# Kernel optimization log

Hardware: AMD Instinct MI355X
Metric: run time of the kernel (lower is better)

## Reference

```python
import jax, jax.numpy as jnp
import numpy as np

B, T = 4096, 2048
CLIP = 1.0e5


def _hv(x):
    # smooth Heaviside: ~0 for x<0, ~1 for x>0
    return (jnp.tanh(5.0 * x) + 1.0) * 0.5


def setup_inputs() -> dict:
    key = jax.random.key(0)
    k1, _ = jax.random.split(key)
    # columns: prcp, tmean, dayl (all in [0,1) like normalized forcings)
    inputs = jax.random.uniform(k1, (B, T, 3), dtype=jnp.float32)
    # 15 scalar bucket parameters, all initialized to 0.5 as in build():
    # f, smax, qmax, ddf, tmin, tmax, Kc, SCmax, spmax, qpmax, kp, sgmax, qgmax, Kl, Kn
    theta = jnp.full((15,), 0.5, dtype=jnp.float32)
    return {"inputs": inputs, "theta": theta}


def _run(inputs, theta):
    f, smax, qmax, ddf, tmin, tmax, Kc, SCmax, spmax, qpmax, kp, sgmax, qgmax, Kl, Kn = [
        theta[i] for i in range(15)
    ]
    prcp = inputs[:, :, 0]   # [B,T]
    tmean = inputs[:, :, 1]
    dayl = inputs[:, :, 2]
    # Hamon-style PET computed once for the whole sequence
    pet = 29.8 * (dayl * 24.0) * 0.611 * jnp.exp(17.3 * tmean / (tmean + 237.3)) / (tmean + 273.2)

    # rescaled parameters (done once; constant over time)
    f_ = f / 10.0
    smax_ = smax * 1950.0
    qmax_ = qmax * 50.0
    ddf_ = ddf * 5.0
    tmin_ = tmin * -3.0
    tmax_ = tmax * 3.0
    Kc_ = Kc * 0.5
    SCmax_ = SCmax * 1.5
    spmax_ = spmax * 1950.0
    qpmax_ = qpmax * 40.0
    sgmax_ = sgmax * 1950.0
    qgmax_ = qgmax * 40.0
    Kl_ = Kl * 0.5
    Kn_ = Kn * 0.5
    Dc = 0.986 * 0.862

    def step(state, xt):
        s0, s1, s2, s3, s4 = [state[:, i] for i in range(5)]  # each [B]
        p, t, dl, pe = xt  # each [B]

        # canopy bucket
        day = _hv(dl - 0.5)
        night = _hv(0.5 - dl)
        scmax_t = day * SCmax_ * 2.0 + night * SCmax_ * 0.6
        lai_t = day * 0.478 + night * 0.15
        kc_t = day * Kc_ + night * Kc_ * 0.4
        pintc = (_hv(p - 0.1) * _hv(s0) * _hv(s0 - scmax_t) * p
                 + _hv(p - 0.1) * _hv(scmax_t - s0) * kc_t * Dc * lai_t)

        # rain/snow partition
        psnow = _hv(tmin_ - t) * p
        prain = _hv(t - tmin_) * p

        # snow bucket
        melt = _hv(t - tmax_) * _hv(s1) * jnp.minimum(s1, ddf_ * (t - tmax_))

        # preferential bucket
        qpref = (_hv(s2) * _hv(s2 - spmax_) * qpmax_
                 + _hv(s2) * _hv(spmax_ - s2) * kp * p * jnp.exp(-f_ * (spmax_ - s2)))

        # capillary (soil) bucket
        et = (_hv(s3) * _hv(s3 - smax_) * pe
              + _hv(s3) * _hv(smax_ - s3) * pe * (s3 / smax_))
        qsub = (_hv(s3) * _hv(s3 - smax_) * qmax_
                + _hv(s3) * _hv(smax_ - s3) * qmax_ * jnp.exp(-f_ * (smax_ - s3)))
        qout = _hv(s3) * _hv(s3 - smax_) * (s3 - smax_)

        # gravity bucket
        qslow = (_hv(s4) * _hv(s4 - sgmax_) * qgmax_
                 + _hv(s4) * _hv(sgmax_ - s4) * (p * Kl_ + p * p * Kn_) * jnp.exp(-f_ * (sgmax_ - s4)))

        ns0 = s0 + jnp.clip(pintc, -CLIP, CLIP)
        ns1 = s1 + jnp.clip(psnow - melt, -CLIP, CLIP)
        ns2 = s2 + jnp.clip(qpref, -CLIP, CLIP)
        ns3 = s3 + jnp.clip(prain + melt - et - qsub - qout, -CLIP, CLIP)
        ns4 = s4 + jnp.clip(qslow, -CLIP, CLIP)
        new_state = jnp.stack([ns0, ns1, ns2, ns3, ns4], axis=1)  # [B,5]
        return new_state, new_state

    init = jnp.zeros((inputs.shape[0], 5), dtype=inputs.dtype)
    xs = (prcp.T, tmean.T, dayl.T, pet.T)  # time-major [T,B]
    _, seq = jax.lax.scan(step, init, xs)  # seq: [T,B,5]
    return jnp.transpose(seq, (1, 0, 2))  # [B,T,5] state trajectories


def reference(inputs, theta):
    return _run(inputs, theta)
```

## Files before the change

kernel.cpp:

```cpp
#include <hip/hip_runtime.h>


#define NB 4096
#define NT 2048
#define CH 16
#define NCH (NT / CH)
#define CH23 32
#define BT ((size_t)NB * (size_t)NT)

#define L2E10 14.4269504089f
#define L2E    1.44269504089f

__device__ __forceinline__ float rcpf(float x) { return __builtin_amdgcn_rcpf(x); }
__device__ __forceinline__ float ex2(float a)  { return __builtin_amdgcn_exp2f(a); }
__device__ __forceinline__ float ex2c(float a) { return __builtin_amdgcn_exp2f(fminf(a, 80.0f)); }
__device__ __forceinline__ float clip1e5(float x) {
    return __builtin_amdgcn_fmed3f(x, -100000.0f, 100000.0f);
}
__device__ __forceinline__ void pinbuf(const float* d, int n4) {
    const float4* v = (const float4*)d;
    #pragma unroll
    for (int i = 0; i < n4; ++i)
        asm volatile("" :: "v"(v[i].x), "v"(v[i].y), "v"(v[i].z), "v"(v[i].w));
}

__global__ __launch_bounds__(64, 1)
void prnn_roles(const float* __restrict__ inp, const float* __restrict__ theta,
                float* __restrict__ out, float* __restrict__ wsp, int use_ws) {
    const int lane = threadIdx.x;
    const int role = blockIdx.x & 3;
    const int b = (blockIdx.x >> 2) * 64 + lane;

    const float f_     = theta[0] * 0.1f;
    const float smax_  = theta[1] * 1950.0f;
    const float qmax_  = theta[2] * 50.0f;
    const float ddf_   = theta[3] * 5.0f;
    const float tmin_  = theta[4] * -3.0f;
    const float tmax_  = theta[5] * 3.0f;
    const float Kc_    = theta[6] * 0.5f;
    const float SCmax_ = theta[7] * 1.5f;
    const float spmax_ = theta[8] * 1950.0f;
    const float qpmax_ = theta[9] * 40.0f;
    const float kp     = theta[10];
    const float sgmax_ = theta[11] * 1950.0f;
    const float qgmax_ = theta[12] * 40.0f;
    const float Kl_    = theta[13] * 0.5f;
    const float Kn_    = theta[14] * 0.5f;

    const float inv_smax = rcpf(smax_);
    const float KcDc  = Kc_ * 0.849932f;
    const float c_sn  = -L2E10 * tmin_;
    const float c_m   =  L2E10 * tmax_;
    const float c_dd  = -ddf_ * tmax_;
    const float c_sc1 =  L2E10 * SCmax_ * 1.4f;
    const float c_sc0 =  L2E10 * SCmax_ * 0.6f;
    const float c_2p  =  L2E10 * spmax_;
    const float c_3s  =  L2E10 * smax_;
    const float c_4s  =  L2E10 * sgmax_;
    const float fE    = f_ * L2E;
    const float c_E2  = -fE * spmax_;
    const float c_E3  = -fE * smax_;
    const float c_E4  = -fE * sgmax_;

    const float* ip = inp + (size_t)b * (NT * 3);
    float*       op = out + (size_t)b * (NT * 5);
    float* wbase = use_ws ? wsp : out;

    auto plane_storeN = [&](float* plane, const float* ob, int off, int n4) {
        float4* d = (float4*)(plane + (size_t)off);
        const float4* s = (const float4*)ob;
        #pragma unroll
        for (int i = 0; i < 8; ++i) { if (i < n4) d[i] = s[i]; }
    };

    if (role == 0) {
        float s0 = 0.f;
        float* w0 = wbase + 0 * BT + (size_t)b * NT;
        float bA[CH * 3], bB[CH * 3];
        auto pf = [&](float* d, int c) {
            const float4* s = (const float4*)(ip + (size_t)c * (CH * 3));
            #pragma unroll
            for (int i = 0; i < (CH * 3) / 4; ++i) ((float4*)d)[i] = s[i];
        };
        auto cw = [&](const float* d, int c) {
            float ob[CH];
            #pragma unroll
            for (int i = 0; i < CH; ++i) {
                const float p  = d[i * 3 + 0];
                const float dl = d[i * 3 + 2];
                const float day = rcpf(1.0f + ex2(fmaf(-L2E10, dl, 7.21347520f)));
                const float da  = 1.0f + ex2(fmaf(-L2E10, p, L2E));
                const float lai   = fmaf(0.328f, day, 0.15f);
                const float kcf   = fmaf(0.6f, day, 0.4f);
                const float kterm = KcDc * kcf * lai;
                const float zday  = fmaf(c_sc1, day, c_sc0);
                const float e0  = ex2(-L2E10 * s0);
                const float esc = ex2(fmaf(-L2E10, s0, zday));
                const float d0  = 1.0f + e0;
                const float dsc = 1.0f + esc;
                const float Rp  = rcpf(da * d0 * dsc);
                const float pintc = Rp * fmaf(d0 * esc, kterm, p);
                s0 += clip1e5(pintc);
                ob[i] = s0;
            }
            if (use_ws) plane_storeN(w0, ob, c * CH, CH / 4);
            else {
                #pragma unroll
                for (int i = 0; i < CH; ++i) op[(c * CH + i) * 5 + 0] = ob[i];
            }
        };
        pf(bA, 0);
        for (int c = 0; c < NCH; c += 2) {
            pf(bB, c + 1);
            pinbuf(bA, (CH * 3) / 4);
            cw(bA, c);
            if (c + 2 < NCH) pf(bA, c + 2);
            pinbuf(bB, (CH * 3) / 4);
            cw(bB, c + 1);
        }
    } else if (role == 1) {
        float s1 = 0.f, s3 = 0.f;
        float* w1 = wbase + 1 * BT + (size_t)b * NT;
        float* w3 = wbase + 3 * BT + (size_t)b * NT;
        float bA[CH * 3], bB[CH * 3];
        auto pf = [&](float* d, int c) {
            const float4* s = (const float4*)(ip + (size_t)c * (CH * 3));
            #pragma unroll
            for (int i = 0; i < (CH * 3) / 4; ++i) ((float4*)d)[i] = s[i];
        };
        auto cw = [&](const float* d, int c) {
            float ob1[CH], ob3[CH];
            #pragma unroll
            for (int i = 0; i < CH; ++i) {
                const float p  = d[i * 3 + 0];
                const float tm = d[i * 3 + 1];
                const float dl = d[i * 3 + 2];
                const float A1 = tm + 237.3f;
                const float A2 = tm + 273.2f;
                const float qq = rcpf(A1 * A2);
                const float pe = 436.98672f * dl * ex2(24.958624f * tm * (qq * A2)) * (qq * A1);
                const float psnow = rcpf(1.0f + ex2(fmaf(L2E10, tm, c_sn))) * p;
                const float dm = 1.0f + ex2(fmaf(-L2E10, tm, c_m));
                const float prain = p - psnow;
                const float e1 = ex2(-L2E10 * s1);
                const float melt = rcpf(dm * (1.0f + e1))
                                   * fminf(s1, fmaf(ddf_, tm, c_dd));
                const float e3  = ex2(-L2E10 * s3);
                const float e3s = ex2c(fmaf(-L2E10, s3, c_3s));
                const float R3  = rcpf((1.0f + e3) * (1.0f + e3s));
                const float E3  = ex2(fmaf(fE, s3, c_E3));
                const float t_et = pe * fmaf(e3s * s3, inv_smax, 1.0f);
                const float t_qs = qmax_ * fmaf(e3s, E3, 1.0f);
                const float outflux = R3 * (t_et + t_qs + (s3 - smax_));
                const float ds3 = prain + melt - outflux;
                s1 += clip1e5(psnow - melt);
                s3 += clip1e5(ds3);
                ob1[i] = s1;
                ob3[i] = s3;
            }
            if (use_ws) {
                plane_storeN(w1, ob1, c * CH, CH / 4);
                plane_storeN(w3, ob3, c * CH, CH / 4);
            } else {
                #pragma unroll
                for (int i = 0; i < CH; ++i) {
                    op[(c * CH + i) * 5 + 1] = ob1[i];
                    op[(c * CH + i) * 5 + 3] = ob3[i];
                }
            }
        };
        pf(bA, 0);
        for (int c = 0; c < NCH; c += 2) {
            pf(bB, c + 1);
            pinbuf(bA, (CH * 3) / 4);
            cw(bA, c);
            if (c + 2 < NCH) pf(bA, c + 2);
            pinbuf(bB, (CH * 3) / 4);
            cw(bB, c + 1);
        }
    } else if (role == 2) {
        float s2 = 0.f;
        float pA[CH23], pB[CH23];
        float* w2 = wbase + 2 * BT + (size_t)b * NT;
        auto pf = [&](float* P, int c) {
            #pragma unroll
            for (int i = 0; i < CH23; ++i) P[i] = ip[(c * CH23 + i) * 3 + 0];
        };
        auto cw = [&](const float* P, int c) {
            float ob[CH23];
            #pragma unroll
            for (int i = 0; i < CH23; ++i) {
                const float p = P[i];
                const float e2  = ex2(-L2E10 * s2);
                const float e2p = ex2c(fmaf(-L2E10, s2, c_2p));
                const float R2  = rcpf((1.0f + e2) * (1.0f + e2p));
                const float E2  = ex2(fmaf(fE, s2, c_E2));
                const float qpref = R2 * fmaf(e2p * E2, kp * p, qpmax_);
                s2 += clip1e5(qpref);
                ob[i] = s2;
            }
            if (use_ws) plane_storeN(w2, ob, c * CH23, CH23 / 4);
            else {
                #pragma unroll
                for (int i = 0; i < CH23; ++i) op[(c * CH23 + i) * 5 + 2] = ob[i];
            }
        };
        pf(pA, 0);
        for (int c = 0; c < NT / CH23; c += 2) {
            pf(pB, c + 1);
            pinbuf(pA, CH23 / 4);
            cw(pA, c);
            if (c + 2 < NT / CH23) pf(pA, c + 2);
            pinbuf(pB, CH23 / 4);
            cw(pB, c + 1);
        }
    } else {
        float s4 = 0.f;
        float pA[CH23], pB[CH23];
        float* w4 = wbase + 4 * BT + (size_t)b * NT;
        auto pf = [&](float* P, int c) {
            #pragma unroll
            for (int i = 0; i < CH23; ++i) P[i] = ip[(c * CH23 + i) * 3 + 0];
        };
        auto cw = [&](const float* P, int c) {
            float ob[CH23];
            #pragma unroll
            for (int i = 0; i < CH23; ++i) {
                const float p = P[i];
                const float e4  = ex2(-L2E10 * s4);
                const float e4s = ex2c(fmaf(-L2E10, s4, c_4s));
                const float R4  = rcpf((1.0f + e4) * (1.0f + e4s));
                const float E4  = ex2(fmaf(fE, s4, c_E4));
                const float pl  = p * fmaf(p, Kn_, Kl_);
                const float qslow = R4 * fmaf(e4s * E4, pl, qgmax_);
                s4 += clip1e5(qslow);
                ob[i] = s4;
            }
            if (use_ws) plane_storeN(w4, ob, c * CH23, CH23 / 4);
            else {
                #pragma unroll
                for (int i = 0; i < CH23; ++i) op[(c * CH23 + i) * 5 + 4] = ob[i];
            }
        };
        pf(pA, 0);
        for (int c = 0; c < NT / CH23; c += 2) {
            pf(pB, c + 1);
            pinbuf(pA, CH23 / 4);
            cw(pA, c);
            if (c + 2 < NT / CH23) pf(pA, c + 2);
            pinbuf(pB, CH23 / 4);
            cw(pB, c + 1);
        }
    }
}

__global__ __launch_bounds__(256)
void tx_kernel(const float* __restrict__ wsp, float* __restrict__ out) {
    const size_t idx = (size_t)blockIdx.x * 256 + threadIdx.x;
    const size_t b  = idx / (NT / 8);
    const size_t t0 = (idx % (NT / 8)) * 8;
    const float* base = wsp + b * NT + t0;
    float v[5][8];
    #pragma unroll
    for (int s = 0; s < 5; ++s) {
        *(float4*)&v[s][0] = *(const float4*)(base + s * BT);
        *(float4*)&v[s][4] = *(const float4*)(base + s * BT + 4);
    }
    float o[40];
    #pragma unroll
    for (int t = 0; t < 8; ++t)
        #pragma unroll
        for (int s = 0; s < 5; ++s) o[t * 5 + s] = v[s][t];
    float4* d = (float4*)(out + (b * NT + t0) * 5);
    const float4* sv = (const float4*)o;
    #pragma unroll
    for (int i = 0; i < 10; ++i) d[i] = sv[i];
}

extern "C" void kernel_launch(void* const* d_in, const int* in_sizes, int n_in,
                              void* d_out, int out_size, void* d_ws, size_t ws_size,
                              hipStream_t stream) {
    const float* inp   = (const float*)d_in[0];
    const float* theta = (const float*)d_in[1];
    float* out = (float*)d_out;
    float* wsp = (float*)d_ws;
    const int use_ws = (wsp != nullptr && ws_size >= 5 * sizeof(float) * BT) ? 1 : 0;
    prnn_roles<<<4 * (NB / 64), 64, 0, stream>>>(inp, theta, out, wsp, use_ws);
    if (use_ws)
        tx_kernel<<<(int)(BT / 8 / 256), 256, 0, stream>>>(wsp, out);
}
```

Measured before the change: 561.2 us.

## Process two batch rows per thread to interleave independent recurrences

Each thread now advances two independent batch rows' recurrences in lockstep, providing instruction-level parallelism to hide the latency of the serial exp/rcp chain. The grid is halved accordingly, and chunk sizes are unified to 8 timesteps with stores every two chunks. The trade-off is half as many wavefronts across the GPU, leaving many CUs idle, plus higher register pressure.

New measurement: 876.0 us. +56.1%, slower.

```diff
diff --git a/kernel.cpp b/kernel.cpp
--- a/kernel.cpp
+++ b/kernel.cpp
@@ -3,9 +3,8 @@
 
 #define NB 4096
 #define NT 2048
-#define CH 16
+#define CH 8
 #define NCH (NT / CH)
-#define CH23 32
 #define BT ((size_t)NB * (size_t)NT)
 
 #define L2E10 14.4269504089f
@@ -29,7 +28,8 @@
                 float* __restrict__ out, float* __restrict__ wsp, int use_ws) {
     const int lane = threadIdx.x;
     const int role = blockIdx.x & 3;
-    const int b = (blockIdx.x >> 2) * 64 + lane;
+    const int b0 = (blockIdx.x >> 2) * 128 + lane;
+    const int b1 = b0 + 64;
 
     const float f_     = theta[0] * 0.1f;
     const float smax_  = theta[1] * 1950.0f;
@@ -62,194 +62,273 @@
     const float c_E3  = -fE * smax_;
     const float c_E4  = -fE * sgmax_;
 
-    const float* ip = inp + (size_t)b * (NT * 3);
-    float*       op = out + (size_t)b * (NT * 5);
+    const float* ip0 = inp + (size_t)b0 * (NT * 3);
+    const float* ip1 = inp + (size_t)b1 * (NT * 3);
+    float*       op0 = out + (size_t)b0 * (NT * 5);
+    float*       op1 = out + (size_t)b1 * (NT * 5);
     float* wbase = use_ws ? wsp : out;
 
-    auto plane_storeN = [&](float* plane, const float* ob, int off, int n4) {
+    auto st16 = [&](float* plane, const float* ob, int off) {
         float4* d = (float4*)(plane + (size_t)off);
         const float4* s = (const float4*)ob;
         #pragma unroll
-        for (int i = 0; i < 8; ++i) { if (i < n4) d[i] = s[i]; }
+        for (int i = 0; i < 4; ++i) d[i] = s[i];
     };
 
     if (role == 0) {
-        float s0 = 0.f;
-        float* w0 = wbase + 0 * BT + (size_t)b * NT;
-        float bA[CH * 3], bB[CH * 3];
-        auto pf = [&](float* d, int c) {
-            const float4* s = (const float4*)(ip + (size_t)c * (CH * 3));
-            #pragma unroll
-            for (int i = 0; i < (CH * 3) / 4; ++i) ((float4*)d)[i] = s[i];
-        };
-        auto cw = [&](const float* d, int c) {
-            float ob[CH];
-            #pragma unroll
-            for (int i = 0; i < CH; ++i) {
-                const float p  = d[i * 3 + 0];
-                const float dl = d[i * 3 + 2];
-                const float day = rcpf(1.0f + ex2(fmaf(-L2E10, dl, 7.21347520f)));
-                const float da  = 1.0f + ex2(fmaf(-L2E10, p, L2E));
-                const float lai   = fmaf(0.328f, day, 0.15f);
-                const float kcf   = fmaf(0.6f, day, 0.4f);
-                const float kterm = KcDc * kcf * lai;
-                const float zday  = fmaf(c_sc1, day, c_sc0);
-                const float e0  = ex2(-L2E10 * s0);
-                const float esc = ex2(fmaf(-L2E10, s0, zday));
-                const float d0  = 1.0f + e0;
-                const float dsc = 1.0f + esc;
-                const float Rp  = rcpf(da * d0 * dsc);
-                const float pintc = Rp * fmaf(d0 * esc, kterm, p);
-                s0 += clip1e5(pintc);
-                ob[i] = s0;
-            }
-            if (use_ws) plane_storeN(w0, ob, c * CH, CH / 4);
+        float sa = 0.f, sb = 0.f;
+        float iA0[CH * 3], iA1[CH * 3], iB0[CH * 3], iB1[CH * 3];
+        float oa[2 * CH], ob[2 * CH];
+        float* w0a = wbase + 0 * BT + (size_t)b0 * NT;
+        float* w0b = wbase + 0 * BT + (size_t)b1 * NT;
+        auto pf = [&](float* d0, float* d1, int c) {
+            const float4* s0 = (const float4*)(ip0 + (size_t)c * (CH * 3));
+            const float4* s1 = (const float4*)(ip1 + (size_t)c * (CH * 3));
+            #pragma unroll
+            for (int i = 0; i < (CH * 3) / 4; ++i) {
+                ((float4*)d0)[i] = s0[i];
+                ((float4*)d1)[i] = s1[i];
+            }
+        };
+        auto cw = [&](const float* d0, const float* d1, int half) {
+            #pragma unroll
+            for (int i = 0; i < CH; ++i) {
+                const float p0 = d0[i * 3 + 0], p1 = d1[i * 3 + 0];
+                const float dl0 = d0[i * 3 + 2], dl1 = d1[i * 3 + 2];
+                const float dy0 = rcpf(1.0f + ex2(fmaf(-L2E10, dl0, 7.21347520f)));
+                const float dy1 = rcpf(1.0f + ex2(fmaf(-L2E10, dl1, 7.21347520f)));
+                const float da0 = 1.0f + ex2(fmaf(-L2E10, p0, L2E));
+                const float da1 = 1.0f + ex2(fmaf(-L2E10, p1, L2E));
+                const float la0 = fmaf(0.328f, dy0, 0.15f);
+                const float la1 = fmaf(0.328f, dy1, 0.15f);
+                const float kc0 = fmaf(0.6f, dy0, 0.4f);
+                const float kc1 = fmaf(0.6f, dy1, 0.4f);
+                const float kt0 = KcDc * kc0 * la0;
+                const float kt1 = KcDc * kc1 * la1;
+                const float zd0 = fmaf(c_sc1, dy0, c_sc0);
+                const float zd1 = fmaf(c_sc1, dy1, c_sc0);
+                const float e0a = ex2(-L2E10 * sa);
+                const float e0b = ex2(-L2E10 * sb);
+                const float ea  = ex2(fmaf(-L2E10, sa, zd0));
+                const float eb  = ex2(fmaf(-L2E10, sb, zd1));
+                const float d0a = 1.0f + e0a;
+                const float d0b = 1.0f + e0b;
+                const float dsa = 1.0f + ea;
+                const float dsb = 1.0f + eb;
+                const float Ra  = rcpf(da0 * d0a * dsa);
+                const float Rb  = rcpf(da1 * d0b * dsb);
+                const float pa  = Ra * fmaf(d0a * ea, kt0, p0);
+                const float pb  = Rb * fmaf(d0b * eb, kt1, p1);
+                sa += clip1e5(pa);
+                sb += clip1e5(pb);
+                oa[half * CH + i] = sa;
+                ob[half * CH + i] = sb;
+            }
+        };
+        pf(iA0, iA1, 0);
+        for (int c = 0; c < NCH; c += 2) {
+            pf(iB0, iB1, c + 1);
+            pinbuf(iA0, (CH * 3) / 4); pinbuf(iA1, (CH * 3) / 4);
+            cw(iA0, iA1, 0);
+            if (c + 2 < NCH) pf(iA0, iA1, c + 2);
+            pinbuf(iB0, (CH * 3) / 4); pinbuf(iB1, (CH * 3) / 4);
+            cw(iB0, iB1, 1);
+            if (use_ws) { st16(w0a, oa, c * CH); st16(w0b, ob, c * CH); }
             else {
                 #pragma unroll
-                for (int i = 0; i < CH; ++i) op[(c * CH + i) * 5 + 0] = ob[i];
-            }
-        };
-        pf(bA, 0);
-        for (int c = 0; c < NCH; c += 2) {
-            pf(bB, c + 1);
-            pinbuf(bA, (CH * 3) / 4);
-            cw(bA, c);
-            if (c + 2 < NCH) pf(bA, c + 2);
-            pinbuf(bB, (CH * 3) / 4);
-            cw(bB, c + 1);
+                for (int i = 0; i < 2 * CH; ++i) {
+                    op0[(c * CH + i) * 5 + 0] = oa[i];
+                    op1[(c * CH + i) * 5 + 0] = ob[i];
+                }
+            }
         }
     } else if (role == 1) {
-        float s1 = 0.f, s3 = 0.f;
-        float* w1 = wbase + 1 * BT + (size_t)b * NT;
-        float* w3 = wbase + 3 * BT + (size_t)b * NT;
-        float bA[CH * 3], bB[CH * 3];
-        auto pf = [&](float* d, int c) {
-            const float4* s = (const float4*)(ip + (size_t)c * (CH * 3));
-            #pragma unroll
-            for (int i = 0; i < (CH * 3) / 4; ++i) ((float4*)d)[i] = s[i];
-        };
-        auto cw = [&](const float* d, int c) {
-            float ob1[CH], ob3[CH];
-            #pragma unroll
-            for (int i = 0; i < CH; ++i) {
-                const float p  = d[i * 3 + 0];
-                const float tm = d[i * 3 + 1];
-                const float dl = d[i * 3 + 2];
-                const float A1 = tm + 237.3f;
-                const float A2 = tm + 273.2f;
-                const float qq = rcpf(A1 * A2);
-                const float pe = 436.98672f * dl * ex2(24.958624f * tm * (qq * A2)) * (qq * A1);
-                const float psnow = rcpf(1.0f + ex2(fmaf(L2E10, tm, c_sn))) * p;
-                const float dm = 1.0f + ex2(fmaf(-L2E10, tm, c_m));
-                const float prain = p - psnow;
-                const float e1 = ex2(-L2E10 * s1);
-                const float melt = rcpf(dm * (1.0f + e1))
-                                   * fminf(s1, fmaf(ddf_, tm, c_dd));
-                const float e3  = ex2(-L2E10 * s3);
-                const float e3s = ex2c(fmaf(-L2E10, s3, c_3s));
-                const float R3  = rcpf((1.0f + e3) * (1.0f + e3s));
-                const float E3  = ex2(fmaf(fE, s3, c_E3));
-                const float t_et = pe * fmaf(e3s * s3, inv_smax, 1.0f);
-                const float t_qs = qmax_ * fmaf(e3s, E3, 1.0f);
-                const float outflux = R3 * (t_et + t_qs + (s3 - smax_));
-                const float ds3 = prain + melt - outflux;
-                s1 += clip1e5(psnow - melt);
-                s3 += clip1e5(ds3);
-                ob1[i] = s1;
-                ob3[i] = s3;
-            }
+        float s1a = 0.f, s1b = 0.f, s3a = 0.f, s3b = 0.f;
+        float iA0[CH * 3], iA1[CH * 3], iB0[CH * 3], iB1[CH * 3];
+        float o1a[2 * CH], o1b[2 * CH], o3a[2 * CH], o3b[2 * CH];
+        float* w1a = wbase + 1 * BT + (size_t)b0 * NT;
+        float* w1b = wbase + 1 * BT + (size_t)b1 * NT;
+        float* w3a = wbase + 3 * BT + (size_t)b0 * NT;
+        float* w3b = wbase + 3 * BT + (size_t)b1 * NT;
+        auto pf = [&](float* d0, float* d1, int c) {
+            const float4* s0 = (const float4*)(ip0 + (size_t)c * (CH * 3));
+            const float4* s1 = (const float4*)(ip1 + (size_t)c * (CH * 3));
+            #pragma unroll
+            for (int i = 0; i < (CH * 3) / 4; ++i) {
+                ((float4*)d0)[i] = s0[i];
+                ((float4*)d1)[i] = s1[i];
+            }
+        };
+        auto cw = [&](const float* d0, const float* d1, int half) {
+            #pragma unroll
+            for (int i = 0; i < CH; ++i) {
+                const float p0 = d0[i * 3 + 0], p1 = d1[i * 3 + 0];
+                const float t0 = d0[i * 3 + 1], t1 = d1[i * 3 + 1];
+                const float l0 = d0[i * 3 + 2], l1 = d1[i * 3 + 2];
+                const float A1a = t0 + 237.3f, A1b = t1 + 237.3f;
+                const float A2a = t0 + 273.2f, A2b = t1 + 273.2f;
+                const float qa = rcpf(A1a * A2a);
+                const float qb = rcpf(A1b * A2b);
+                const float pea = 436.98672f * l0 * ex2(24.958624f * t0 * (qa * A2a)) * (qa * A1a);
+                const float peb = 436.98672f * l1 * ex2(24.958624f * t1 * (qb * A2b)) * (qb * A1b);
+                const float psa = rcpf(1.0f + ex2(fmaf(L2E10, t0, c_sn))) * p0;
+                const float psb = rcpf(1.0f + ex2(fmaf(L2E10, t1, c_sn))) * p1;
+                const float dma = 1.0f + ex2(fmaf(-L2E10, t0, c_m));
+                const float dmb = 1.0f + ex2(fmaf(-L2E10, t1, c_m));
+                const float pra = p0 - psa;
+                const float prb = p1 - psb;
+                const float e1a = ex2(-L2E10 * s1a);
+                const float e1b = ex2(-L2E10 * s1b);
+                const float mla = rcpf(dma * (1.0f + e1a)) * fminf(s1a, fmaf(ddf_, t0, c_dd));
+                const float mlb = rcpf(dmb * (1.0f + e1b)) * fminf(s1b, fmaf(ddf_, t1, c_dd));
+                const float e3a = ex2(-L2E10 * s3a);
+                const float e3b = ex2(-L2E10 * s3b);
+                const float ga  = ex2c(fmaf(-L2E10, s3a, c_3s));
+                const float gb  = ex2c(fmaf(-L2E10, s3b, c_3s));
+                const float Ra  = rcpf((1.0f + e3a) * (1.0f + ga));
+                const float Rb  = rcpf((1.0f + e3b) * (1.0f + gb));
+                const float Ea  = ex2(fmaf(fE, s3a, c_E3));
+                const float Eb  = ex2(fmaf(fE, s3b, c_E3));
+                const float ta_ = pea * fmaf(ga * s3a, inv_smax, 1.0f);
+                const float tb_ = peb * fmaf(gb * s3b, inv_smax, 1.0f);
+                const float ua  = qmax_ * fmaf(ga, Ea, 1.0f);
+                const float ub  = qmax_ * fmaf(gb, Eb, 1.0f);
+                const float ofa = Ra * (ta_ + ua + (s3a - smax_));
+                const float ofb = Rb * (tb_ + ub + (s3b - smax_));
+                const float d3a = pra + mla - ofa;
+                const float d3b = prb + mlb - ofb;
+                s1a += clip1e5(psa - mla);
+                s1b += clip1e5(psb - mlb);
+                s3a += clip1e5(d3a);
+                s3b += clip1e5(d3b);
+                o1a[half * CH + i] = s1a;
+                o1b[half * CH + i] = s1b;
+                o3a[half * CH + i] = s3a;
+                o3b[half * CH + i] = s3b;
+            }
+        };
+        pf(iA0, iA1, 0);
+        for (int c = 0; c < NCH; c += 2) {
+            pf(iB0, iB1, c + 1);
+            pinbuf(iA0, (CH * 3) / 4); pinbuf(iA1, (CH * 3) / 4);
+            cw(iA0, iA1, 0);
+            if (c + 2 < NCH) pf(iA0, iA1, c + 2);
+            pinbuf(iB0, (CH * 3) / 4); pinbuf(iB1, (CH * 3) / 4);
+            cw(iB0, iB1, 1);
             if (use_ws) {
-                plane_storeN(w1, ob1, c * CH, CH / 4);
-                plane_storeN(w3, ob3, c * CH, CH / 4);
+                st16(w1a, o1a, c * CH); st16(w1b, o1b, c * CH);
+                st16(w3a, o3a, c * CH); st16(w3b, o3b, c * CH);
             } else {
                 #pragma unroll
-                for (int i = 0; i < CH; ++i) {
-                    op[(c * CH + i) * 5 + 1] = ob1[i];
-                    op[(c * CH + i) * 5 + 3] = ob3[i];
+                for (int i = 0; i < 2 * CH; ++i) {
+                    op0[(c * CH + i) * 5 + 1] = o1a[i];
+                    op1[(c * CH + i) * 5 + 1] = o1b[i];
+                    op0[(c * CH + i) * 5 + 3] = o3a[i];
+                    op1[(c * CH + i) * 5 + 3] = o3b[i];
                 }
             }
-        };
-        pf(bA, 0);
-        for (int c = 0; c < NCH; c += 2) {
-            pf(bB, c + 1);
-            pinbuf(bA, (CH * 3) / 4);
-            cw(bA, c);
-            if (c + 2 < NCH) pf(bA, c + 2);
-            pinbuf(bB, (CH * 3) / 4);
-            cw(bB, c + 1);
         }
     } else if (role == 2) {
-        float s2 = 0.f;
-        float pA[CH23], pB[CH23];
-        float* w2 = wbase + 2 * BT + (size_t)b * NT;
-        auto pf = [&](float* P, int c) {
-            #pragma unroll
-            for (int i = 0; i < CH23; ++i) P[i] = ip[(c * CH23 + i) * 3 + 0];
-        };
-        auto cw = [&](const float* P, int c) {
-            float ob[CH23];
-            #pragma unroll
-            for (int i = 0; i < CH23; ++i) {
-                const float p = P[i];
-                const float e2  = ex2(-L2E10 * s2);
-                const float e2p = ex2c(fmaf(-L2E10, s2, c_2p));
-                const float R2  = rcpf((1.0f + e2) * (1.0f + e2p));
-                const float E2  = ex2(fmaf(fE, s2, c_E2));
-                const float qpref = R2 * fmaf(e2p * E2, kp * p, qpmax_);
-                s2 += clip1e5(qpref);
-                ob[i] = s2;
-            }
-            if (use_ws) plane_storeN(w2, ob, c * CH23, CH23 / 4);
+        float sa = 0.f, sb = 0.f;
+        float pA0[CH], pA1[CH], pB0[CH], pB1[CH];
+        float oa[2 * CH], ob[2 * CH];
+        float* w2a = wbase + 2 * BT + (size_t)b0 * NT;
+        float* w2b = wbase + 2 * BT + (size_t)b1 * NT;
+        auto pf = [&](float* P0, float* P1, int c) {
+            #pragma unroll
+            for (int i = 0; i < CH; ++i) {
+                P0[i] = ip0[(c * CH + i) * 3 + 0];
+                P1[i] = ip1[(c * CH + i) * 3 + 0];
+            }
+        };
+        auto cw = [&](const float* P0, const float* P1, int half) {
+            #pragma unroll
+            for (int i = 0; i < CH; ++i) {
+                const float p0 = P0[i], p1 = P1[i];
+                const float e2a = ex2(-L2E10 * sa);
+                const float e2b = ex2(-L2E10 * sb);
+                const float ga  = ex2c(fmaf(-L2E10, sa, c_2p));
+                const float gb  = ex2c(fmaf(-L2E10, sb, c_2p));
+                const float Ra  = rcpf((1.0f + e2a) * (1.0f + ga));
+                const float Rb  = rcpf((1.0f + e2b) * (1.0f + gb));
+                const float Ea  = ex2(fmaf(fE, sa, c_E2));
+                const float Eb  = ex2(fmaf(fE, sb, c_E2));
+                const float qa  = Ra * fmaf(ga * Ea, kp * p0, qpmax_);
+                const float qb  = Rb * fmaf(gb * Eb, kp * p1, qpmax_);
+                sa += clip1e5(qa);
+                sb += clip1e5(qb);
+                oa[half * CH + i] = sa;
+                ob[half * CH + i] = sb;
+            }
+        };
+        pf(pA0, pA1, 0);
+        for (int c = 0; c < NCH; c += 2) {
+            pf(pB0, pB1, c + 1);
+            pinbuf(pA0, CH / 4); pinbuf(pA1, CH / 4);
+            cw(pA0, pA1, 0);
+            if (c + 2 < NCH) pf(pA0, pA1, c + 2);
+            pinbuf(pB0, CH / 4); pinbuf(pB1, CH / 4);
+            cw(pB0, pB1, 1);
+            if (use_ws) { st16(w2a, oa, c * CH); st16(w2b, ob, c * CH); }
             else {
                 #pragma unroll
-                for (int i = 0; i < CH23; ++i) op[(c * CH23 + i) * 5 + 2] = ob[i];
-            }
-        };
-        pf(pA, 0);
-        for (int c = 0; c < NT / CH23; c += 2) {
-            pf(pB, c + 1);
-            pinbuf(pA, CH23 / 4);
-            cw(pA, c);
-            if (c + 2 < NT / CH23) pf(pA, c + 2);
-            pinbuf(pB, CH23 / 4);
-            cw(pB, c + 1);
+                for (int i = 0; i < 2 * CH; ++i) {
+                    op0[(c * CH + i) * 5 + 2] = oa[i];
+                    op1[(c * CH + i) * 5 + 2] = ob[i];
+                }
+            }
         }
     } else {
-        float s4 = 0.f;
-        float pA[CH23], pB[CH23];
-        float* w4 = wbase + 4 * BT + (size_t)b * NT;
-        auto pf = [&](float* P, int c) {
-            #pragma unroll
-            for (int i = 0; i < CH23; ++i) P[i] = ip[(c * CH23 + i) * 3 + 0];
-        };
-        auto cw = [&](const float* P, int c) {
-            float ob[CH23];
-            #pragma unroll
-            for (int i = 0; i < CH23; ++i) {
-                const float p = P[i];
-                const float e4  = ex2(-L2E10 * s4);
-                const float e4s = ex2c(fmaf(-L2E10, s4, c_4s));
-                const float R4  = rcpf((1.0f + e4) * (1.0f + e4s));
-                const float E4  = ex2(fmaf(fE, s4, c_E4));
-                const float pl  = p * fmaf(p, Kn_, Kl_);
-                const float qslow = R4 * fmaf(e4s * E4, pl, qgmax_);
-                s4 += clip1e5(qslow);
-                ob[i] = s4;
-            }
-            if (use_ws) plane_storeN(w4, ob, c * CH23, CH23 / 4);
+        float sa = 0.f, sb = 0.f;
+        float pA0[CH], pA1[CH], pB0[CH], pB1[CH];
+        float oa[2 * CH], ob[2 * CH];
+        float* w4a = wbase + 4 * BT + (size_t)b0 * NT;
+        float* w4b = wbase + 4 * BT + (size_t)b1 * NT;
+        auto pf = [&](float* P0, float* P1, int c) {
+            #pragma unroll
+            for (int i = 0; i < CH; ++i) {
+                P0[i] = ip0[(c * CH + i) * 3 + 0];
+                P1[i] = ip1[(c * CH + i) * 3 + 0];
+            }
+        };
+        auto cw = [&](const float* P0, const float* P1, int half) {
+            #pragma unroll
+            for (int i = 0; i < CH; ++i) {
+                const float p0 = P0[i], p1 = P1[i];
+                const float e4a = ex2(-L2E10 * sa);
+                const float e4b = ex2(-L2E10 * sb);
+                const float ga  = ex2c(fmaf(-L2E10, sa, c_4s));
+                const float gb  = ex2c(fmaf(-L2E10, sb, c_4s));
+                const float Ra  = rcpf((1.0f + e4a) * (1.0f + ga));
+                const float Rb  = rcpf((1.0f + e4b) * (1.0f + gb));
+                const float Ea  = ex2(fmaf(fE, sa, c_E4));
+                const float Eb  = ex2(fmaf(fE, sb, c_E4));
+                const float pl0 = p0 * fmaf(p0, Kn_, Kl_);
+                const float pl1 = p1 * fmaf(p1, Kn_, Kl_);
+                const float qa  = Ra * fmaf(ga * Ea, pl0, qgmax_);
+                const float qb  = Rb * fmaf(gb * Eb, pl1, qgmax_);
+                sa += clip1e5(qa);
+                sb += clip1e5(qb);
+                oa[half * CH + i] = sa;
+                ob[half * CH + i] = sb;
+            }
+        };
+        pf(pA0, pA1, 0);
+        for (int c = 0; c < NCH; c += 2) {
+            pf(pB0, pB1, c + 1);
+            pinbuf(pA0, CH / 4); pinbuf(pA1, CH / 4);
+            cw(pA0, pA1, 0);
+            if (c + 2 < NCH) pf(pA0, pA1, c + 2);
+            pinbuf(pB0, CH / 4); pinbuf(pB1, CH / 4);
+            cw(pB0, pB1, 1);
+            if (use_ws) { st16(w4a, oa, c * CH); st16(w4b, ob, c * CH); }
             else {
                 #pragma unroll
-                for (int i = 0; i < CH23; ++i) op[(c * CH23 + i) * 5 + 4] = ob[i];
-            }
-        };
-        pf(pA, 0);
-        for (int c = 0; c < NT / CH23; c += 2) {
-            pf(pB, c + 1);
-            pinbuf(pA, CH23 / 4);
-            cw(pA, c);
-            if (c + 2 < NT / CH23) pf(pA, c + 2);
-            pinbuf(pB, CH23 / 4);
-            cw(pB, c + 1);
+                for (int i = 0; i < 2 * CH; ++i) {
+                    op0[(c * CH + i) * 5 + 4] = oa[i];
+                    op1[(c * CH + i) * 5 + 4] = ob[i];
+                }
+            }
         }
     }
 }
@@ -285,7 +364,7 @@
     float* out = (float*)d_out;
     float* wsp = (float*)d_ws;
     const int use_ws = (wsp != nullptr && ws_size >= 5 * sizeof(float) * BT) ? 1 : 0;
-    prnn_roles<<<4 * (NB / 64), 64, 0, stream>>>(inp, theta, out, wsp, use_ws);
+    prnn_roles<<<4 * (NB / 128), 64, 0, stream>>>(inp, theta, out, wsp, use_ws);
     if (use_ws)
         tx_kernel<<<(int)(BT / 8 / 256), 256, 0, stream>>>(wsp, out);
 }
```
